# Kernel optimization log

Hardware: AMD Instinct MI355X
Metric: run time of the kernel (lower is better)

Reference implementation:

```python
import jax, jax.numpy as jnp
import numpy as np

N_NODES = 100000
HIDDEN = 64
IN_CH = 128
N_EDGES = 1600000


def setup_inputs() -> dict:
    key = jax.random.key(0)
    ks = jax.random.split(key, 12)
    x = jax.random.normal(ks[0], (N_NODES, IN_CH), dtype=jnp.float32)
    edge_index = jax.random.randint(ks[1], (2, N_EDGES), 0, N_NODES, dtype=jnp.int64)

    def glorot(k, fan_in, fan_out):
        s = jnp.sqrt(6.0 / (fan_in + fan_out)).astype(jnp.float32)
        return jax.random.uniform(k, (fan_in, fan_out), jnp.float32, -s, s)

    return {
        "x": x,
        "edge_index": edge_index,
        # GCNConv layer 1: linear (no bias) + post-aggregation bias
        "W1": glorot(ks[2], IN_CH, HIDDEN),
        "b1": jnp.zeros((HIDDEN,), jnp.float32),
        # GCNConv layer 2
        "W2": glorot(ks[3], HIDDEN, HIDDEN),
        "b2": jnp.zeros((HIDDEN,), jnp.float32),
        # edge classifier MLP: Linear(2H,H) -> ReLU -> Linear(H,2)
        "Wc1": glorot(ks[4], 2 * HIDDEN, HIDDEN),
        "bc1": jnp.zeros((HIDDEN,), jnp.float32),
        "Wc2": glorot(ks[5], HIDDEN, 2),
        "bc2": jnp.zeros((2,), jnp.float32),
    }


def _gcn_forward(x, edge_index, W1, b1, W2, b2, Wc1, bc1, Wc2, bc2):
    n = x.shape[0]
    src, dst = edge_index[0], edge_index[1]
    # add self-loops (PyG GCNConv default)
    loop = jnp.arange(n, dtype=edge_index.dtype)
    a_src = jnp.concatenate([src, loop])  # [E+N]
    a_dst = jnp.concatenate([dst, loop])
    # symmetric normalization: deg over destination with unit edge weights
    deg = jax.ops.segment_sum(jnp.ones(a_dst.shape[0], x.dtype), a_dst, num_segments=n)
    dis = jax.lax.rsqrt(deg)  # deg >= 1 due to self-loops
    norm = dis[a_src] * dis[a_dst]  # [E+N]

    def conv(h, W, b):
        h = h @ W  # [N, H]
        msg = h[a_src] * norm[:, None]  # [E+N, H] gather + scale
        return jax.ops.segment_sum(msg, a_dst, num_segments=n) + b

    h = jax.nn.relu(conv(x, W1, b1))  # dropout is identity in eval mode
    h = conv(h, W2, b2)
    # edge classifier on concatenated endpoint embeddings
    e = jnp.concatenate([h[src], h[dst]], axis=1)  # [E, 2H]
    z = jax.nn.relu(e @ Wc1 + bc1)
    return z @ Wc2 + bc2  # [E, 2]


def reference(x, edge_index, W1, b1, W2, b2, Wc1, bc1, Wc2, bc2):
    return _gcn_forward(x, edge_index, W1, b1, W2, b2, Wc1, bc1, Wc2, bc2)
```

## Files before the change

kernel.cpp:

```cpp
#include <hip/hip_runtime.h>
#include <hip/hip_fp16.h>

#define HID 64
#define BKT_SHIFT 10
#define BKT_NODES 1024
#define PCHUNKS 512

typedef _Float16 half8 __attribute__((ext_vector_type(8)));
typedef _Float16 half4 __attribute__((ext_vector_type(4)));
typedef float f32x4 __attribute__((ext_vector_type(4)));

__global__ __launch_bounds__(256) void k_bkt_count(const int* __restrict__ dst,
                                                   int* __restrict__ G, int E,
                                                   int nbkt, int chunk) {
  __shared__ int hist[128];
  int p = blockIdx.x, tid = threadIdx.x;
  for (int i = tid; i < nbkt; i += 256) hist[i] = 0;
  __syncthreads();
  int s = p * chunk, e = min(s + chunk, E);
  for (int i = s + tid; i < e; i += 256) atomicAdd(&hist[dst[i] >> BKT_SHIFT], 1);
  __syncthreads();
  for (int b = tid; b < nbkt; b += 256) G[b * PCHUNKS + p] = hist[b];
}

__global__ void k_scan1(const int* __restrict__ in, int* __restrict__ scanout,
                        int* __restrict__ blocksums, int n) {
  __shared__ int sdata[256];
  int tid = threadIdx.x;
  int base = blockIdx.x * 1024 + tid * 4;
  int v0 = 0, v1 = 0, v2 = 0, v3 = 0;
  if (base + 0 < n) v0 = in[base + 0];
  if (base + 1 < n) v1 = in[base + 1];
  if (base + 2 < n) v2 = in[base + 2];
  if (base + 3 < n) v3 = in[base + 3];
  int tsum = v0 + v1 + v2 + v3;
  sdata[tid] = tsum;
  __syncthreads();
  for (int off = 1; off < 256; off <<= 1) {
    int t = (tid >= off) ? sdata[tid - off] : 0;
    __syncthreads();
    sdata[tid] += t;
    __syncthreads();
  }
  int excl = sdata[tid] - tsum;
  if (base + 0 < n) scanout[base + 0] = excl;
  if (base + 1 < n) scanout[base + 1] = excl + v0;
  if (base + 2 < n) scanout[base + 2] = excl + v0 + v1;
  if (base + 3 < n) scanout[base + 3] = excl + v0 + v1 + v2;
  if (tid == 255) blocksums[blockIdx.x] = sdata[255];
}

__global__ void k_scan2(int* blocksums, int nb) {
  __shared__ int s[128];
  int tid = threadIdx.x;
  int v = (tid < nb) ? blocksums[tid] : 0;
  s[tid] = v;
  __syncthreads();
  for (int off = 1; off < 128; off <<= 1) {
    int t = (tid >= off) ? s[tid - off] : 0;
    __syncthreads();
    s[tid] += t;
    __syncthreads();
  }
  if (tid < nb) blocksums[tid] = s[tid] - v;
}

__global__ void k_scan3(const int* __restrict__ scanout,
                        const int* __restrict__ blocksums, int* __restrict__ outp,
                        int n) {
  int i = blockIdx.x * blockDim.x + threadIdx.x;
  if (i < n) outp[i] = scanout[i] + blocksums[i >> 10];
}

__global__ __launch_bounds__(256) void k_bkt_scatter(
    const int* __restrict__ src, const int* __restrict__ dst,
    const int* __restrict__ Gscan, int* __restrict__ psrc,
    unsigned short* __restrict__ pdst, int E, int nbkt, int chunk) {
  __shared__ int gbase[128];
  __shared__ int rcnt[128];
  int p = blockIdx.x, tid = threadIdx.x;
  for (int b = tid; b < nbkt; b += 256) {
    gbase[b] = Gscan[b * PCHUNKS + p];
    rcnt[b] = 0;
  }
  __syncthreads();
  int s = p * chunk, e = min(s + chunk, E);
  for (int i = s + tid; i < e; i += 256) {
    int d = dst[i];
    int b = d >> BKT_SHIFT;
    int r = atomicAdd(&rcnt[b], 1);
    int pos = gbase[b] + r;
    psrc[pos] = src[i];
    pdst[pos] = (unsigned short)(d & (BKT_NODES - 1));
  }
}

__global__ __launch_bounds__(1024) void k_bkt_final(
    const int* __restrict__ Gscan, const int* __restrict__ psrc,
    const unsigned short* __restrict__ pdst, int* __restrict__ rowoff,
    float* __restrict__ dis, int* __restrict__ csr_src, int E, int nbkt, int N) {
  __shared__ int cnt[BKT_NODES];
  __shared__ int lo[BKT_NODES];
  int b = blockIdx.x, tid = threadIdx.x;
  int s = Gscan[b * PCHUNKS];
  int eend = (b + 1 < nbkt) ? Gscan[(b + 1) * PCHUNKS] : E;
  cnt[tid] = 0;
  __syncthreads();
  for (int i = s + tid; i < eend; i += 1024) atomicAdd(&cnt[pdst[i]], 1);
  __syncthreads();
  int v = cnt[tid];
  lo[tid] = v;
  __syncthreads();
  for (int off = 1; off < 1024; off <<= 1) {
    int t = (tid >= off) ? lo[tid - off] : 0;
    __syncthreads();
    lo[tid] += t;
    __syncthreads();
  }
  int excl = lo[tid] - v;
  int node = b * BKT_NODES + tid;
  if (node < N) {
    rowoff[node] = s + excl;
    dis[node] = rsqrtf((float)v + 1.0f);
  }
  __syncthreads();
  lo[tid] = excl;
  cnt[tid] = 0;
  __syncthreads();
  for (int i = s + tid; i < eend; i += 1024) {
    int ln = pdst[i];
    int r = atomicAdd(&cnt[ln], 1);
    csr_src[s + lo[ln] + r] = psrc[i];
  }
}

__global__ void k_pack_all(const float* __restrict__ W1, const float* __restrict__ W2,
                           const float* __restrict__ Wc1, const float* __restrict__ bc1,
                           __half* __restrict__ packW1, __half* __restrict__ packW2,
                           __half* __restrict__ packUV, float* __restrict__ biasUV,
                           __half* __restrict__ ysent) {
  int b = blockIdx.x, tid = threadIdx.x;
  if (b < 4) {
    int t = b * 256 + tid;
    int f = t >> 6, L = t & 63;
    int kc = f >> 2, nb = f & 3;
    int k = 32 * kc + ((L >> 4) << 3);
    int n = (L & 15) + 16 * nb;
    for (int j = 0; j < 8; ++j)
      packW1[(t << 3) + j] = __float2half(W1[(k + j) * 64 + n]);
  } else if (b < 6) {
    int t = (b - 4) * 256 + tid;
    int f = t >> 6, L = t & 63;
    int kc = f >> 2, nb = f & 3;
    int k = 32 * kc + ((L >> 4) << 3);
    int n = (L & 15) + 16 * nb;
    for (int j = 0; j < 8; ++j)
      packW2[(t << 3) + j] = __float2half(W2[(k + j) * 64 + n]);
  } else if (b < 10) {
    int t = (b - 6) * 256 + tid;
    int f = t >> 6, L = t & 63;
    int kc = f >> 3, nb = f & 7;
    int k = 32 * kc + ((L >> 4) << 3);
    int n = (L & 15) + 16 * nb;
    for (int j = 0; j < 8; ++j) {
      float w = (n < 64) ? Wc1[(k + j) * 64 + n] : Wc1[(64 + k + j) * 64 + (n - 64)];
      packUV[(t << 3) + j] = __float2half(w);
    }
  } else {
    if (tid < 128) biasUV[tid] = (tid < 64) ? bc1[tid] : 0.f;
    else if (tid < 192) ysent[tid - 128] = __float2half(0.f);
  }
}

template <int K, int NOUT, bool F32IN>
__global__ __launch_bounds__(256) void k_lin_mfma(
    const void* __restrict__ Xv, const __half* __restrict__ packB,
    const float* __restrict__ bias, const float* __restrict__ dis,
    __half* __restrict__ Y, int n) {
  int wid = blockIdx.x * 4 + (threadIdx.x >> 6);
  int rowbase = wid * 16;
  if (rowbase >= n) return;
  int L = threadIdx.x & 63;
  int m16 = L & 15, quad = L >> 4;
  constexpr int KC = K / 32;
  constexpr int NB = NOUT / 16;

  half8 Bf[KC * NB];
  const half8* packv = (const half8*)packB;
#pragma unroll
  for (int f = 0; f < KC * NB; ++f) Bf[f] = packv[f * 64 + L];

  int r = min(rowbase + m16, n - 1);
  half8 Af[KC];
  if (F32IN) {
    const float* xr = (const float*)Xv + (long)r * K;
#pragma unroll
    for (int kc = 0; kc < KC; ++kc) {
      const float4* xp = (const float4*)(xr + kc * 32 + quad * 8);
      float4 a = xp[0], b = xp[1];
      half8 v = {(_Float16)a.x, (_Float16)a.y, (_Float16)a.z, (_Float16)a.w,
                 (_Float16)b.x, (_Float16)b.y, (_Float16)b.z, (_Float16)b.w};
      Af[kc] = v;
    }
  } else {
    const half8* xr = (const half8*)((const __half*)Xv + (long)r * K);
#pragma unroll
    for (int kc = 0; kc < KC; ++kc) Af[kc] = xr[kc * 4 + quad];
  }

  f32x4 acc[NB];
#pragma unroll
  for (int nb = 0; nb < NB; ++nb) acc[nb] = {0.f, 0.f, 0.f, 0.f};
#pragma unroll
  for (int kc = 0; kc < KC; ++kc)
#pragma unroll
    for (int nb = 0; nb < NB; ++nb)
      acc[nb] = __builtin_amdgcn_mfma_f32_16x16x32_f16(Af[kc], Bf[kc * NB + nb],
                                                       acc[nb], 0, 0, 0);

  float dv[4];
#pragma unroll
  for (int j = 0; j < 4; ++j) {
    int ro = rowbase + quad * 4 + j;
    dv[j] = (dis && ro < n) ? dis[ro] : 1.f;
  }
#pragma unroll
  for (int nb = 0; nb < NB; ++nb) {
    int col = m16 + 16 * nb;
    float bv = bias ? bias[col] : 0.f;
#pragma unroll
    for (int j = 0; j < 4; ++j) {
      int ro = rowbase + quad * 4 + j;
      if (ro < n) {
        float v = (acc[nb][j] + bv) * dv[j];
        Y[(long)ro * NOUT + col] = __float2half(v);
      }
    }
  }
}

__global__ __launch_bounds__(256) void k_agg_csr(
    const __half* __restrict__ Yh, const float* __restrict__ dis,
    const int* __restrict__ rowoff, const int* __restrict__ csr_src,
    const float* __restrict__ b, __half* __restrict__ A, int n, int E, int relu) {
  int node = blockIdx.x * 4 + (threadIdx.x >> 6);
  if (node >= n) return;
  int L = threadIdx.x & 63;
  int sub = L >> 4;
  int cq = L & 15;
  const half4* Y4 = (const half4*)Yh;
  float dd = dis[node];
  int i0 = rowoff[node];
  int end = (node == n - 1) ? E : rowoff[node + 1];

  float z[4][4] = {{0.f}};
  if (sub == 0) {
    half4 hv = Y4[(long)node * 16 + cq];
#pragma unroll
    for (int j = 0; j < 4; ++j) z[0][j] = (float)hv[j];
  }

  int last = end - 1;
  for (int base = i0; base < end; base += 16) {
    int sidx[4];
#pragma unroll
    for (int slot = 0; slot < 4; ++slot) {
      int idx = base + slot * 4 + sub;
      int sl = csr_src[min(idx, last)];
      sidx[slot] = (idx < end) ? sl : n;
    }
#pragma unroll
    for (int slot = 0; slot < 4; ++slot) {
      half4 hv = Y4[(long)sidx[slot] * 16 + cq];
#pragma unroll
      for (int j = 0; j < 4; ++j) z[slot][j] += (float)hv[j];
    }
  }

  float a[4];
#pragma unroll
  for (int j = 0; j < 4; ++j) {
    a[j] = (z[0][j] + z[1][j]) + (z[2][j] + z[3][j]);
    a[j] += __shfl_xor(a[j], 16, 64);
    a[j] += __shfl_xor(a[j], 32, 64);
  }
  if (sub == 0) {
    float4 bb = ((const float4*)b)[cq];
    float v0 = fmaf(a[0], dd, bb.x), v1 = fmaf(a[1], dd, bb.y);
    float v2 = fmaf(a[2], dd, bb.z), v3 = fmaf(a[3], dd, bb.w);
    if (relu) {
      v0 = fmaxf(v0, 0.f); v1 = fmaxf(v1, 0.f);
      v2 = fmaxf(v2, 0.f); v3 = fmaxf(v3, 0.f);
    }
    half4 o = {(_Float16)v0, (_Float16)v1, (_Float16)v2, (_Float16)v3};
    ((half4*)A)[(long)node * 16 + cq] = o;
  }
}

__global__ __launch_bounds__(256) void k_edge_mlp(
    const __half* __restrict__ UV, const int* __restrict__ src,
    const int* __restrict__ dst, const float* __restrict__ Wc2,
    const float* __restrict__ bc2, float* __restrict__ out, int E, int nwaves) {
  int wid = blockIdx.x * 4 + (threadIdx.x >> 6);
  int L = threadIdx.x & 63;
  int sub = L >> 4;
  int cq = L & 15;

  float w0[4], w1[4];
#pragma unroll
  for (int j = 0; j < 4; ++j) {
    int c = cq * 4 + j;
    w0[j] = Wc2[2 * c];
    w1[j] = Wc2[2 * c + 1];
  }
  float ob0 = bc2[0], ob1 = bc2[1];

  const half4* UV4 = (const half4*)UV;
  int last = E - 1;

  for (long base = (long)wid * 32; base < E; base += (long)nwaves * 32) {
    int se[8], de[8];
#pragma unroll
    for (int slot = 0; slot < 8; ++slot) {
      int e = (int)base + slot * 4 + sub;
      int ec = min(e, last);
      se[slot] = src[ec];
      de[slot] = dst[ec];
    }
    half4 uu[8], vv[8];
#pragma unroll
    for (int slot = 0; slot < 8; ++slot) {
      uu[slot] = UV4[(long)se[slot] * 32 + cq];
      vv[slot] = UV4[(long)de[slot] * 32 + 16 + cq];
    }
#pragma unroll
    for (int slot = 0; slot < 8; ++slot) {
      float o0 = 0.f, o1 = 0.f;
#pragma unroll
      for (int j = 0; j < 4; ++j) {
        float v = fmaxf((float)uu[slot][j] + (float)vv[slot][j], 0.f);
        o0 = fmaf(v, w0[j], o0);
        o1 = fmaf(v, w1[j], o1);
      }
      o0 += __shfl_xor(o0, 1, 64);
      o1 += __shfl_xor(o1, 1, 64);
      o0 += __shfl_xor(o0, 2, 64);
      o1 += __shfl_xor(o1, 2, 64);
      o0 += __shfl_xor(o0, 4, 64);
      o1 += __shfl_xor(o1, 4, 64);
      o0 += __shfl_xor(o0, 8, 64);
      o1 += __shfl_xor(o1, 8, 64);
      int e = (int)base + slot * 4 + sub;
      if (cq == 0 && e < E) {
        float2 o = {o0 + ob0, o1 + ob1};
        *(float2*)(out + 2 * (long)e) = o;
      }
    }
  }
}

extern "C" void kernel_launch(void* const* d_in, const int* in_sizes, int n_in,
                              void* d_out, int out_size, void* d_ws, size_t ws_size,
                              hipStream_t stream) {
  const float* x   = (const float*)d_in[0];
  const int*   ei  = (const int*)d_in[1];
  const float* W1  = (const float*)d_in[2];
  const float* b1  = (const float*)d_in[3];
  const float* W2  = (const float*)d_in[4];
  const float* b2  = (const float*)d_in[5];
  const float* Wc1 = (const float*)d_in[6];
  const float* bc1 = (const float*)d_in[7];
  const float* Wc2 = (const float*)d_in[8];
  const float* bc2 = (const float*)d_in[9];

  const int N = in_sizes[0] / 128;
  const int E = in_sizes[1] / 2;
  const int* src = ei;
  const int* dst = ei + E;

  const int nbkt = (N + BKT_NODES - 1) >> BKT_SHIFT;
  const int gsz = nbkt * PCHUNKS;
  const int chunk = (E + PCHUNKS - 1) / PCHUNKS;

  float* dis     = (float*)d_ws;
  __half* y      = (__half*)(dis + N);
  __half* h      = y + (long)(N + 1) * HID;
  __half* UV     = h + (long)N * HID;
  __half* packW1 = UV + (long)N * 128;
  __half* packW2 = packW1 + 8192;
  __half* packUV = packW2 + 4096;
  float* biasUV  = (float*)(packUV + 8192);
  int* rowoff    = (int*)(biasUV + 128);
  int* csr_src   = rowoff + N;
  int* G         = csr_src + E;
  int* Gs1       = G + gsz;
  int* Gbs       = Gs1 + gsz;
  int* Gscan     = Gbs + 128;
  int* psrc            = (int*)UV;
  unsigned short* pdst = (unsigned short*)(psrc + E);

  const int B = 256;
  int nbScan = (gsz + 1023) / 1024;

  k_pack_all<<<11, B, 0, stream>>>(W1, W2, Wc1, bc1, packW1, packW2, packUV,
                                   biasUV, y + (long)N * HID);
  k_bkt_count<<<PCHUNKS, B, 0, stream>>>(dst, G, E, nbkt, chunk);
  k_scan1<<<nbScan, B, 0, stream>>>(G, Gs1, Gbs, gsz);
  k_scan2<<<1, 128, 0, stream>>>(Gbs, nbScan);
  k_scan3<<<(gsz + B - 1) / B, B, 0, stream>>>(Gs1, Gbs, Gscan, gsz);
  k_bkt_scatter<<<PCHUNKS, B, 0, stream>>>(src, dst, Gscan, psrc, pdst, E, nbkt,
                                           chunk);
  k_bkt_final<<<nbkt, 1024, 0, stream>>>(Gscan, psrc, pdst, rowoff, dis, csr_src,
                                         E, nbkt, N);

  int gAgg = (N + 3) / 4;
  int gLin = (N + 63) / 64;

  k_lin_mfma<128, 64, true><<<gLin, B, 0, stream>>>(x, packW1, nullptr, dis, y, N);
  k_agg_csr<<<gAgg, B, 0, stream>>>(y, dis, rowoff, csr_src, b1, h, N, E, 1);

  k_lin_mfma<64, 64, false><<<gLin, B, 0, stream>>>(h, packW2, nullptr, dis, y, N);
  k_agg_csr<<<gAgg, B, 0, stream>>>(y, dis, rowoff, csr_src, b2, h, N, E, 0);

  k_lin_mfma<64, 128, false><<<gLin, B, 0, stream>>>(h, packUV, biasUV, nullptr, UV, N);
  int cblocks = 2048;
  int nwaves = cblocks * 4;
  k_edge_mlp<<<cblocks, B, 0, stream>>>(UV, src, dst, Wc2, bc2,
                                        (float*)d_out, E, nwaves);
}
```

Baseline: 343.1 us.

## Process edge MLP in destination-bucketed order for V-row gather locality

The bucket scatter now also stores full destination IDs and original edge indices in separate workspace buffers, no longer aliased onto UV. The edge MLP walks edges in dst-bucketed order, with each wave taking a contiguous 128-edge range, so V-row gathers for a dst bucket stay local in cache. Outputs are scattered back to their original edge positions. The cost is wider scatter writes (two int arrays instead of a ushort), extra index reads in the MLP, and scattered 8-byte output stores instead of coalesced ones.

```diff
diff --git a/kernel.cpp b/kernel.cpp
--- a/kernel.cpp
+++ b/kernel.cpp
@@ -75,7 +75,8 @@
 __global__ __launch_bounds__(256) void k_bkt_scatter(
     const int* __restrict__ src, const int* __restrict__ dst,
     const int* __restrict__ Gscan, int* __restrict__ psrc,
-    unsigned short* __restrict__ pdst, int E, int nbkt, int chunk) {
+    int* __restrict__ pdstI, int* __restrict__ peid, int E, int nbkt,
+    int chunk) {
   __shared__ int gbase[128];
   __shared__ int rcnt[128];
   int p = blockIdx.x, tid = threadIdx.x;
@@ -91,13 +92,14 @@
     int r = atomicAdd(&rcnt[b], 1);
     int pos = gbase[b] + r;
     psrc[pos] = src[i];
-    pdst[pos] = (unsigned short)(d & (BKT_NODES - 1));
+    pdstI[pos] = d;
+    peid[pos] = i;
   }
 }
 
 __global__ __launch_bounds__(1024) void k_bkt_final(
     const int* __restrict__ Gscan, const int* __restrict__ psrc,
-    const unsigned short* __restrict__ pdst, int* __restrict__ rowoff,
+    const int* __restrict__ pdstI, int* __restrict__ rowoff,
     float* __restrict__ dis, int* __restrict__ csr_src, int E, int nbkt, int N) {
   __shared__ int cnt[BKT_NODES];
   __shared__ int lo[BKT_NODES];
@@ -106,7 +108,8 @@
   int eend = (b + 1 < nbkt) ? Gscan[(b + 1) * PCHUNKS] : E;
   cnt[tid] = 0;
   __syncthreads();
-  for (int i = s + tid; i < eend; i += 1024) atomicAdd(&cnt[pdst[i]], 1);
+  for (int i = s + tid; i < eend; i += 1024)
+    atomicAdd(&cnt[pdstI[i] & (BKT_NODES - 1)], 1);
   __syncthreads();
   int v = cnt[tid];
   lo[tid] = v;
@@ -128,7 +131,7 @@
   cnt[tid] = 0;
   __syncthreads();
   for (int i = s + tid; i < eend; i += 1024) {
-    int ln = pdst[i];
+    int ln = pdstI[i] & (BKT_NODES - 1);
     int r = atomicAdd(&cnt[ln], 1);
     csr_src[s + lo[ln] + r] = psrc[i];
   }
@@ -297,11 +300,15 @@
   }
 }
 
-__global__ __launch_bounds__(256) void k_edge_mlp(
-    const __half* __restrict__ UV, const int* __restrict__ src,
-    const int* __restrict__ dst, const float* __restrict__ Wc2,
-    const float* __restrict__ bc2, float* __restrict__ out, int E, int nwaves) {
+__global__ __launch_bounds__(256) void k_edge_mlp_part(
+    const __half* __restrict__ UV, const int* __restrict__ psrc,
+    const int* __restrict__ pdstI, const int* __restrict__ peid,
+    const float* __restrict__ Wc2, const float* __restrict__ bc2,
+    float* __restrict__ out, int E, int per) {
   int wid = blockIdx.x * 4 + (threadIdx.x >> 6);
+  long start = (long)wid * per;
+  if (start >= E) return;
+  int stop = (int)min((long)E, start + per);
   int L = threadIdx.x & 63;
   int sub = L >> 4;
   int cq = L & 15;
@@ -316,16 +323,17 @@
   float ob0 = bc2[0], ob1 = bc2[1];
 
   const half4* UV4 = (const half4*)UV;
-  int last = E - 1;
-
-  for (long base = (long)wid * 32; base < E; base += (long)nwaves * 32) {
-    int se[8], de[8];
+  int last = stop - 1;
+
+  for (int base = (int)start; base < stop; base += 32) {
+    int se[8], de[8], ee[8];
 #pragma unroll
     for (int slot = 0; slot < 8; ++slot) {
-      int e = (int)base + slot * 4 + sub;
+      int e = base + slot * 4 + sub;
       int ec = min(e, last);
-      se[slot] = src[ec];
-      de[slot] = dst[ec];
+      se[slot] = psrc[ec];
+      de[slot] = pdstI[ec];
+      ee[slot] = peid[ec];
     }
     half4 uu[8], vv[8];
 #pragma unroll
@@ -350,10 +358,10 @@
       o1 += __shfl_xor(o1, 4, 64);
       o0 += __shfl_xor(o0, 8, 64);
       o1 += __shfl_xor(o1, 8, 64);
-      int e = (int)base + slot * 4 + sub;
-      if (cq == 0 && e < E) {
+      int e = base + slot * 4 + sub;
+      if (cq == 0 && e < stop) {
         float2 o = {o0 + ob0, o1 + ob1};
-        *(float2*)(out + 2 * (long)e) = o;
+        *(float2*)(out + 2 * (long)ee[slot]) = o;
       }
     }
   }
@@ -396,8 +404,9 @@
   int* Gs1       = G + gsz;
   int* Gbs       = Gs1 + gsz;
   int* Gscan     = Gbs + 128;
-  int* psrc            = (int*)UV;
-  unsigned short* pdst = (unsigned short*)(psrc + E);
+  int* psrc      = Gscan + gsz;
+  int* pdstI     = psrc + E;
+  int* peid      = pdstI + E;
 
   const int B = 256;
   int nbScan = (gsz + 1023) / 1024;
@@ -408,9 +417,9 @@
   k_scan1<<<nbScan, B, 0, stream>>>(G, Gs1, Gbs, gsz);
   k_scan2<<<1, 128, 0, stream>>>(Gbs, nbScan);
   k_scan3<<<(gsz + B - 1) / B, B, 0, stream>>>(Gs1, Gbs, Gscan, gsz);
-  k_bkt_scatter<<<PCHUNKS, B, 0, stream>>>(src, dst, Gscan, psrc, pdst, E, nbkt,
-                                           chunk);
-  k_bkt_final<<<nbkt, 1024, 0, stream>>>(Gscan, psrc, pdst, rowoff, dis, csr_src,
+  k_bkt_scatter<<<PCHUNKS, B, 0, stream>>>(src, dst, Gscan, psrc, pdstI, peid,
+                                           E, nbkt, chunk);
+  k_bkt_final<<<nbkt, 1024, 0, stream>>>(Gscan, psrc, pdstI, rowoff, dis, csr_src,
                                          E, nbkt, N);
 
   int gAgg = (N + 3) / 4;
@@ -423,8 +432,9 @@
   k_agg_csr<<<gAgg, B, 0, stream>>>(y, dis, rowoff, csr_src, b2, h, N, E, 0);
 
   k_lin_mfma<64, 128, false><<<gLin, B, 0, stream>>>(h, packUV, biasUV, nullptr, UV, N);
-  int cblocks = 2048;
-  int nwaves = cblocks * 4;
-  k_edge_mlp<<<cblocks, B, 0, stream>>>(UV, src, dst, Wc2, bc2,
-                                        (float*)d_out, E, nwaves);
-}
+  int per = 128;
+  int nw = (E + per - 1) / per;
+  int cblocks = (nw + 3) / 4;
+  k_edge_mlp_part<<<cblocks, B, 0, stream>>>(UV, psrc, pdstI, peid, Wc2, bc2,
+                                             (float*)d_out, E, per);
+}
```

Result: slower. 366.0 us (+6.7%).

## Compute edge MLP first layer per edge with MFMA instead of per-node UV precompute

Applied to the files above, without the earlier changes.

Removes the per-node UV linear kernel and the gather of 128-wide UV rows. Each edge now gathers its two 64-wide hidden rows and runs the concatenated 2H->H layer per edge on MFMA, fusing bias, ReLU and the H->2 output layer. This trades per-node precompute and larger gathers for about sixteen times more matmul FLOPs on the edges. Index loads and output stores become nontemporal, and the loop drops its tail clamp, so E is assumed to be a multiple of 16.

```diff
diff --git a/kernel.cpp b/kernel.cpp
--- a/kernel.cpp
+++ b/kernel.cpp
@@ -9,6 +9,7 @@
 typedef _Float16 half8 __attribute__((ext_vector_type(8)));
 typedef _Float16 half4 __attribute__((ext_vector_type(4)));
 typedef float f32x4 __attribute__((ext_vector_type(4)));
+typedef float f32x2 __attribute__((ext_vector_type(2)));
 
 __global__ __launch_bounds__(256) void k_bkt_count(const int* __restrict__ dst,
                                                    int* __restrict__ G, int E,
@@ -297,64 +298,79 @@
   }
 }
 
-__global__ __launch_bounds__(256) void k_edge_mlp(
-    const __half* __restrict__ UV, const int* __restrict__ src,
-    const int* __restrict__ dst, const float* __restrict__ Wc2,
+__global__ __launch_bounds__(256) void k_edge_mfma(
+    const __half* __restrict__ H, const __half* __restrict__ packUV,
+    const int* __restrict__ src, const int* __restrict__ dst,
+    const float* __restrict__ bc1, const float* __restrict__ Wc2,
     const float* __restrict__ bc2, float* __restrict__ out, int E, int nwaves) {
   int wid = blockIdx.x * 4 + (threadIdx.x >> 6);
   int L = threadIdx.x & 63;
-  int sub = L >> 4;
-  int cq = L & 15;
-
-  float w0[4], w1[4];
-#pragma unroll
-  for (int j = 0; j < 4; ++j) {
-    int c = cq * 4 + j;
-    w0[j] = Wc2[2 * c];
-    w1[j] = Wc2[2 * c + 1];
+  int m16 = L & 15, quad = L >> 4;
+
+  half8 Bf[16];
+  const half8* packv = (const half8*)packUV;
+#pragma unroll
+  for (int f = 0; f < 16; ++f) Bf[f] = packv[f * 64 + L];
+
+  float bcv[4], w0[4], w1[4];
+#pragma unroll
+  for (int nb = 0; nb < 4; ++nb) {
+    int c = m16 + 16 * nb;
+    bcv[nb] = bc1[c];
+    w0[nb] = Wc2[2 * c];
+    w1[nb] = Wc2[2 * c + 1];
   }
   float ob0 = bc2[0], ob1 = bc2[1];
 
-  const half4* UV4 = (const half4*)UV;
-  int last = E - 1;
-
-  for (long base = (long)wid * 32; base < E; base += (long)nwaves * 32) {
-    int se[8], de[8];
-#pragma unroll
-    for (int slot = 0; slot < 8; ++slot) {
-      int e = (int)base + slot * 4 + sub;
-      int ec = min(e, last);
-      se[slot] = src[ec];
-      de[slot] = dst[ec];
-    }
-    half4 uu[8], vv[8];
-#pragma unroll
-    for (int slot = 0; slot < 8; ++slot) {
-      uu[slot] = UV4[(long)se[slot] * 32 + cq];
-      vv[slot] = UV4[(long)de[slot] * 32 + 16 + cq];
-    }
-#pragma unroll
-    for (int slot = 0; slot < 8; ++slot) {
-      float o0 = 0.f, o1 = 0.f;
+  const half8* H8 = (const half8*)H;
+
+  for (long base = (long)wid * 16; base < E; base += (long)nwaves * 16) {
+    int e = (int)base + m16;
+    int se = __builtin_nontemporal_load(&src[e]);
+    int de = __builtin_nontemporal_load(&dst[e]);
+    half8 As0 = H8[(long)se * 8 + quad];
+    half8 As1 = H8[(long)se * 8 + 4 + quad];
+    half8 Ad0 = H8[(long)de * 8 + quad];
+    half8 Ad1 = H8[(long)de * 8 + 4 + quad];
+
+    f32x4 acc[4];
+#pragma unroll
+    for (int nb = 0; nb < 4; ++nb) acc[nb] = {0.f, 0.f, 0.f, 0.f};
+#pragma unroll
+    for (int nb = 0; nb < 4; ++nb) {
+      acc[nb] = __builtin_amdgcn_mfma_f32_16x16x32_f16(As0, Bf[nb], acc[nb], 0, 0, 0);
+      acc[nb] = __builtin_amdgcn_mfma_f32_16x16x32_f16(As1, Bf[8 + nb], acc[nb], 0, 0, 0);
+      acc[nb] = __builtin_amdgcn_mfma_f32_16x16x32_f16(Ad0, Bf[4 + nb], acc[nb], 0, 0, 0);
+      acc[nb] = __builtin_amdgcn_mfma_f32_16x16x32_f16(Ad1, Bf[12 + nb], acc[nb], 0, 0, 0);
+    }
+
+    float o0[4] = {0.f, 0.f, 0.f, 0.f}, o1[4] = {0.f, 0.f, 0.f, 0.f};
+#pragma unroll
+    for (int nb = 0; nb < 4; ++nb) {
 #pragma unroll
       for (int j = 0; j < 4; ++j) {
-        float v = fmaxf((float)uu[slot][j] + (float)vv[slot][j], 0.f);
-        o0 = fmaf(v, w0[j], o0);
-        o1 = fmaf(v, w1[j], o1);
+        float z = fmaxf(acc[nb][j] + bcv[nb], 0.f);
+        o0[j] = fmaf(z, w0[nb], o0[j]);
+        o1[j] = fmaf(z, w1[nb], o1[j]);
       }
-      o0 += __shfl_xor(o0, 1, 64);
-      o1 += __shfl_xor(o1, 1, 64);
-      o0 += __shfl_xor(o0, 2, 64);
-      o1 += __shfl_xor(o1, 2, 64);
-      o0 += __shfl_xor(o0, 4, 64);
-      o1 += __shfl_xor(o1, 4, 64);
-      o0 += __shfl_xor(o0, 8, 64);
-      o1 += __shfl_xor(o1, 8, 64);
-      int e = (int)base + slot * 4 + sub;
-      if (cq == 0 && e < E) {
-        float2 o = {o0 + ob0, o1 + ob1};
-        *(float2*)(out + 2 * (long)e) = o;
-      }
+    }
+#pragma unroll
+    for (int j = 0; j < 4; ++j) {
+      o0[j] += __shfl_xor(o0[j], 1, 64);
+      o1[j] += __shfl_xor(o1[j], 1, 64);
+      o0[j] += __shfl_xor(o0[j], 2, 64);
+      o1[j] += __shfl_xor(o1[j], 2, 64);
+      o0[j] += __shfl_xor(o0[j], 4, 64);
+      o1[j] += __shfl_xor(o1[j], 4, 64);
+      o0[j] += __shfl_xor(o0[j], 8, 64);
+      o1[j] += __shfl_xor(o1[j], 8, 64);
+    }
+    if (m16 == 0) {
+      long eb = base + quad * 4;
+      f32x4 oa = {o0[0] + ob0, o1[0] + ob1, o0[1] + ob0, o1[1] + ob1};
+      f32x4 ob_ = {o0[2] + ob0, o1[2] + ob1, o0[3] + ob0, o1[3] + ob1};
+      __builtin_nontemporal_store(oa, (f32x4*)(out + 2 * eb));
+      __builtin_nontemporal_store(ob_, (f32x4*)(out + 2 * eb + 4));
     }
   }
 }
@@ -422,9 +438,8 @@
   k_lin_mfma<64, 64, false><<<gLin, B, 0, stream>>>(h, packW2, nullptr, dis, y, N);
   k_agg_csr<<<gAgg, B, 0, stream>>>(y, dis, rowoff, csr_src, b2, h, N, E, 0);
 
-  k_lin_mfma<64, 128, false><<<gLin, B, 0, stream>>>(h, packUV, biasUV, nullptr, UV, N);
   int cblocks = 2048;
   int nwaves = cblocks * 4;
-  k_edge_mlp<<<cblocks, B, 0, stream>>>(UV, src, dst, Wc2, bc2,
-                                        (float*)d_out, E, nwaves);
-}
+  k_edge_mfma<<<cblocks, B, 0, stream>>>(h, packUV, src, dst, bc1, Wc2, bc2,
+                                         (float*)d_out, E, nwaves);
+}
```

After: 360.5 us. +5.1%, slower.
